# Optimization experiments

Measured on AMD Instinct MI355X. Metric: run time of the kernel, lower is better.

## Reference

```python
import jax, jax.numpy as jnp
import numpy as np

B, T, L, E = 4, 256, 128, 64  # batch, sample_size (frames), num_harmonies, embedding_size


def setup_inputs() -> dict:
    key = jax.random.key(0)
    k1, k2 = jax.random.split(key)
    return {
        "note_embedding": jax.random.normal(k1, (B, T, E), dtype=jnp.float32),
        "harmony_embedding": jax.random.normal(k2, (B, L, E), dtype=jnp.float32),
    }


def reference(note_embedding, harmony_embedding):
    """SegmentScore.forward: for every segment [s, e] (s <= e), attend the harmony
    embeddings (queries, [B,L,E]) over the note embeddings in that segment
    (keys/values) with scaled dot-product softmax, then score = <harmony, attended>.
    Equivalent closed form: score[b,s,e,l] =
        sum_{t=s..e} softmax_t(raw[b,l,s:e+1])[t] * dot[b,l,t]
    where dot = <harmony_l, note_t> and raw = dot / sqrt(E).
    Vectorized via cumulative sums over the end index for each start index.
    Output: [B, T, T, L]; entries with e < s are 0 (matching torch zeros init).
    """
    scale = 1.0 / jnp.sqrt(jnp.asarray(E, note_embedding.dtype))
    dot = jnp.einsum("ble,bte->blt", harmony_embedding, note_embedding)  # [B,L,T]
    raw = dot * scale
    t_idx = jnp.arange(T)

    def body(carry, s):
        valid = t_idx >= s                                  # [T]
        masked = jnp.where(valid, raw, -jnp.inf)            # [B,L,T]
        m = jnp.max(masked, axis=-1, keepdims=True)         # stable softmax max over t>=s
        exps = jnp.exp(masked - m)                          # 0 where invalid
        denom = jnp.cumsum(exps, axis=-1)                   # running normalizer over e
        numer = jnp.cumsum(exps * dot, axis=-1)             # running <harmony, attended>
        row = jnp.where(valid, numer / jnp.maximum(denom, 1e-30), 0.0)  # [B,L,T_e]
        return carry, row

    _, rows = jax.lax.scan(body, None, t_idx)               # [T_s, B, L, T_e]
    return jnp.transpose(rows, (1, 0, 3, 2))                # [B, T_s, T_e, L]
```

## Files before the change

kernel.cpp:

```cpp
#include <hip/hip_runtime.h>
#include <hip/hip_bf16.h>

#define BB 4
#define TT 256
#define LL 128
#define EE 64
#define SCALE 0.125f

__global__ __launch_bounds__(128) void k_dot(const float* __restrict__ note,
                                             const float* __restrict__ harm,
                                             float* __restrict__ dotT) {
    int bt = blockIdx.x;
    int b = bt >> 8;
    int t = bt & 255;
    int l = threadIdx.x;

    __shared__ float n[EE];
    if (threadIdx.x < EE) n[threadIdx.x] = note[(b * TT + t) * EE + threadIdx.x];
    __syncthreads();

    const float* h = harm + (b * LL + l) * EE;
    float acc = 0.f;
#pragma unroll
    for (int e = 0; e < EE; e += 4) {
        float4 hv = *(const float4*)(h + e);
        acc += hv.x * n[e] + hv.y * n[e + 1] + hv.z * n[e + 2] + hv.w * n[e + 3];
    }
    dotT[(b * TT + t) * LL + l] = acc;
}

__global__ __launch_bounds__(256) void k_sufmax(const float* __restrict__ dotT,
                                                float* __restrict__ MT) {
    int bl = blockIdx.x;
    int b = bl >> 7;
    int l = bl & 127;
    int t = threadIdx.x;

    __shared__ float sm[TT];
    sm[t] = dotT[(b * TT + t) * LL + l] * SCALE;
    __syncthreads();

#pragma unroll
    for (int off = 1; off < TT; off <<= 1) {
        float v = sm[t];
        float o = (t + off < TT) ? sm[t + off] : -3.402823466e38f;
        __syncthreads();
        sm[t] = fmaxf(v, o);
        __syncthreads();
    }
    MT[(b * LL + l) * TT + t] = sm[t];
}

__global__ __launch_bounds__(256) void k_main(const float* __restrict__ dotT,
                                              const float* __restrict__ MT,
                                              float* __restrict__ out) {
    int blk = blockIdx.x;
    int b = blk >> 7;
    int sp = blk & 127;
    int s = sp * 2 + (threadIdx.x >> 7);
    int l = threadIdx.x & 127;

    float m = MT[(b * LL + l) * TT + s];
    const float* dp = dotT + b * TT * LL + l;
    float* op = out + (size_t)((b * TT + s) * TT) * LL + l;

#pragma unroll 8
    for (int e = 0; e < s; ++e) op[e * LL] = 0.f;

    float denom = 0.f, numer = 0.f;
#pragma unroll 4
    for (int e = s; e < TT; ++e) {
        float d = dp[e * LL];
        float ex = __expf(d * SCALE - m);
        denom += ex;
        numer += ex * d;
        op[e * LL] = numer / fmaxf(denom, 1e-30f);
    }
}

extern "C" void kernel_launch(void* const* d_in, const int* in_sizes, int n_in,
                              void* d_out, int out_size, void* d_ws, size_t ws_size,
                              hipStream_t stream) {
    const float* note = (const float*)d_in[0];
    const float* harm = (const float*)d_in[1];
    float* out = (float*)d_out;

    float* dotT = (float*)d_ws;
    float* MT = dotT + BB * TT * LL;

    k_dot<<<BB * TT, 128, 0, stream>>>(note, harm, dotT);
    k_sufmax<<<BB * LL, 256, 0, stream>>>(dotT, MT);
    k_main<<<BB * TT / 2, 256, 0, stream>>>(dotT, MT, out);
}
```

Measured before the change: 152.8 us.

## Replace per-start scans with global-max prefix sums and parallel differencing

```diff
diff --git a/kernel.cpp b/kernel.cpp
--- a/kernel.cpp
+++ b/kernel.cpp
@@ -7,74 +7,90 @@
 #define EE 64
 #define SCALE 0.125f
 
-__global__ __launch_bounds__(128) void k_dot(const float* __restrict__ note,
-                                             const float* __restrict__ harm,
-                                             float* __restrict__ dotT) {
-    int bt = blockIdx.x;
-    int b = bt >> 8;
-    int t = bt & 255;
-    int l = threadIdx.x;
+__global__ __launch_bounds__(256) void k_prefix(const float* __restrict__ note,
+                                                const float* __restrict__ harm,
+                                                double2* __restrict__ P) {
+    int b = blockIdx.x >> 7;
+    int l = blockIdx.x & 127;
+    int t = threadIdx.x;
 
-    __shared__ float n[EE];
-    if (threadIdx.x < EE) n[threadIdx.x] = note[(b * TT + t) * EE + threadIdx.x];
+    __shared__ __align__(16) float h[EE];
+    if (t < EE) h[t] = harm[(b * LL + l) * EE + t];
     __syncthreads();
 
-    const float* h = harm + (b * LL + l) * EE;
+    const float4* n4 = (const float4*)(note + (b * TT + t) * EE);
+    const float4* h4 = (const float4*)h;
     float acc = 0.f;
 #pragma unroll
-    for (int e = 0; e < EE; e += 4) {
-        float4 hv = *(const float4*)(h + e);
-        acc += hv.x * n[e] + hv.y * n[e + 1] + hv.z * n[e + 2] + hv.w * n[e + 3];
+    for (int i = 0; i < EE / 4; ++i) {
+        float4 nv = n4[i];
+        float4 hv = h4[i];
+        acc += nv.x * hv.x + nv.y * hv.y + nv.z * hv.z + nv.w * hv.w;
     }
-    dotT[(b * TT + t) * LL + l] = acc;
+    float dot = acc;
+    float raw = dot * SCALE;
+
+    __shared__ float red[256];
+    red[t] = raw;
+    __syncthreads();
+#pragma unroll
+    for (int off = 128; off > 0; off >>= 1) {
+        if (t < off) red[t] = fmaxf(red[t], red[t + off]);
+        __syncthreads();
+    }
+    float M = red[0];
+    __syncthreads();
+
+    float ex = __expf(raw - M);
+    double vd = (double)ex;
+    double vn = (double)ex * (double)dot;
+
+    __shared__ double sd[TT], sn[TT];
+    sd[t] = vd;
+    sn[t] = vn;
+    __syncthreads();
+#pragma unroll
+    for (int off = 1; off < TT; off <<= 1) {
+        double pd = 0.0, pn = 0.0;
+        if (t >= off) { pd = sd[t - off]; pn = sn[t - off]; }
+        __syncthreads();
+        vd += pd;
+        vn += pn;
+        sd[t] = vd;
+        sn[t] = vn;
+        __syncthreads();
+    }
+
+    P[(b * TT + t) * LL + l] = make_double2(vd, vn);
 }
 
-__global__ __launch_bounds__(256) void k_sufmax(const float* __restrict__ dotT,
-                                                float* __restrict__ MT) {
-    int bl = blockIdx.x;
-    int b = bl >> 7;
-    int l = bl & 127;
-    int t = threadIdx.x;
+__global__ __launch_bounds__(256) void k_out(const double2* __restrict__ P,
+                                             float* __restrict__ out) {
+    int blk = blockIdx.x;
+    int et = blk & 31;
+    int s  = (blk >> 5) & 255;
+    int b  = blk >> 13;
+    int l  = threadIdx.x & 127;
+    int eo = threadIdx.x >> 7;
 
-    __shared__ float sm[TT];
-    sm[t] = dotT[(b * TT + t) * LL + l] * SCALE;
-    __syncthreads();
+    double2 Ps = make_double2(0.0, 0.0);
+    if (s > 0) Ps = P[(b * TT + (s - 1)) * LL + l];
+
+    int e0 = et * 8 + eo * 4;
+    float* op = out + (size_t)(((b * TT + s) * TT) + e0) * LL + l;
+    const double2* pp = P + (b * TT + e0) * LL + l;
 
 #pragma unroll
-    for (int off = 1; off < TT; off <<= 1) {
-        float v = sm[t];
-        float o = (t + off < TT) ? sm[t + off] : -3.402823466e38f;
-        __syncthreads();
-        sm[t] = fmaxf(v, o);
-        __syncthreads();
-    }
-    MT[(b * LL + l) * TT + t] = sm[t];
-}
-
-__global__ __launch_bounds__(256) void k_main(const float* __restrict__ dotT,
-                                              const float* __restrict__ MT,
-                                              float* __restrict__ out) {
-    int blk = blockIdx.x;
-    int b = blk >> 7;
-    int sp = blk & 127;
-    int s = sp * 2 + (threadIdx.x >> 7);
-    int l = threadIdx.x & 127;
-
-    float m = MT[(b * LL + l) * TT + s];
-    const float* dp = dotT + b * TT * LL + l;
-    float* op = out + (size_t)((b * TT + s) * TT) * LL + l;
-
-#pragma unroll 8
-    for (int e = 0; e < s; ++e) op[e * LL] = 0.f;
-
-    float denom = 0.f, numer = 0.f;
-#pragma unroll 4
-    for (int e = s; e < TT; ++e) {
-        float d = dp[e * LL];
-        float ex = __expf(d * SCALE - m);
-        denom += ex;
-        numer += ex * d;
-        op[e * LL] = numer / fmaxf(denom, 1e-30f);
+    for (int k = 0; k < 4; ++k) {
+        int e = e0 + k;
+        float r = 0.f;
+        if (e >= s) {
+            double2 Pe = pp[k * LL];
+            float den = (float)(Pe.x - Ps.x);
+            float num = (float)(Pe.y - Ps.y);
+            r = __fdividef(num, fmaxf(den, 1e-30f));
+        }
+        op[k * LL] = r;
     }
 }
 
@@ -85,10 +101,8 @@
     const float* harm = (const float*)d_in[1];
     float* out = (float*)d_out;
 
-    float* dotT = (float*)d_ws;
-    float* MT = dotT + BB * TT * LL;
+    double2* P = (double2*)d_ws;
 
-    k_dot<<<BB * TT, 128, 0, stream>>>(note, harm, dotT);
-    k_sufmax<<<BB * LL, 256, 0, stream>>>(dotT, MT);
-    k_main<<<BB * TT / 2, 256, 0, stream>>>(dotT, MT, out);
+    k_prefix<<<BB * LL, 256, 0, stream>>>(note, harm, P);
+    k_out<<<BB * TT * 32, 256, 0, stream>>>(P, out);
 }
```

Result: no change. 153.6 us (+0.6%).
